# Optimization experiments

Measured on AMD Instinct MI355X. Metric: run time of the kernel, lower is better.

## Reference

```python
import jax, jax.numpy as jnp
import numpy as np

D = 2048      # feature dim (fc1 = Linear(2*2048, 2048))
S = 10240


def setup_inputs() -> dict:
    key = jax.random.key(0)
    ks = jax.random.split(key, 16)
    sc = 0.02
    z = lambda *s: jnp.zeros(s, jnp.float32)
    return {
        "x0": jax.random.normal(ks[0], (1, 1, D), jnp.float32),
        "x1": jax.random.normal(ks[1], (1, S, D), jnp.float32),
        # fc1: Linear(4096, 2048)  (stored input-major for x @ W)
        "W1": jax.random.normal(ks[2], (2 * D, D), jnp.float32) * sc,
        "b1": z(D),
        # fc2: Linear(2048, 1)
        "W2": jax.random.normal(ks[3], (D, 1), jnp.float32) * sc,
        "b2": z(1),
        # LSTM(input=1, hidden=1, bidirectional): per-direction gate params [4] = (i,f,g,o)
        "Wih_f": jax.random.normal(ks[4], (4,), jnp.float32) * 0.5,
        "Whh_f": jax.random.normal(ks[5], (4,), jnp.float32) * 0.5,
        "bih_f": z(4),
        "bhh_f": z(4),
        "Wih_b": jax.random.normal(ks[6], (4,), jnp.float32) * 0.5,
        "Whh_b": jax.random.normal(ks[7], (4,), jnp.float32) * 0.5,
        "bih_b": z(4),
        "bhh_b": z(4),
        # fc3: Linear(10, 1)
        "W3": jax.random.normal(ks[8], (10, 1), jnp.float32) * sc,
        "b3": z(1),
    }


def _lstm_dir(x_seq, Wih, Whh, bih, bhh):
    """Single-direction LSTM, input_size=hidden_size=1, batch=1.
    x_seq: [S] scalars. Returns h sequence [S]. PyTorch gate order (i,f,g,o)."""
    b = bih + bhh

    def step(carry, x):
        h, c = carry
        g = Wih * x + Whh * h + b              # [4]
        i = jax.nn.sigmoid(g[0])
        f = jax.nn.sigmoid(g[1])
        gg = jnp.tanh(g[2])
        o = jax.nn.sigmoid(g[3])
        c = f * c + i * gg
        h = o * jnp.tanh(c)
        return (h, c), h

    h0 = jnp.zeros((), x_seq.dtype)
    c0 = jnp.zeros((), x_seq.dtype)
    _, hs = jax.lax.scan(step, (h0, c0), x_seq)
    return hs


def reference(x0, x1, W1, b1, W2, b2,
              Wih_f, Whh_f, bih_f, bhh_f,
              Wih_b, Whh_b, bih_b, bhh_b,
              W3, b3):
    # similarity: cat(|x0 - x1|, x0 + x1) along features (x0 broadcasts over S)
    sim = jnp.concatenate([jnp.abs(x0 - x1), x0 + x1], axis=2)   # [1, S, 2D]
    h = jax.nn.relu(jnp.einsum('bsf,fd->bsd', sim, W1) + b1)     # [1, S, D]
    # (dropout is identity in eval mode)
    s = jax.nn.sigmoid(jnp.einsum('bsd,do->bso', h, W2) + b2)    # [1, S, 1]
    x_seq = s[0, :, 0]                                           # [S]

    h_f = _lstm_dir(x_seq, Wih_f, Whh_f, bih_f, bhh_f)           # [S]
    h_b = _lstm_dir(x_seq[::-1], Wih_b, Whh_b, bih_b, bhh_b)[::-1]
    out = jnp.stack([h_f, h_b], axis=1)                          # [S, 2] == lstm out [S,1,2]

    grp = out.reshape(1, -1, 10)                                 # [1, S*2/10, 10]
    y = jax.nn.sigmoid(grp @ W3 + b3)                            # [1, S*2/10, 1]
    return y.reshape(1, -1)
```

## Files before the change

### kernel.cpp

```cpp
#include <hip/hip_runtime.h>
#include <hip/hip_bf16.h>

#define DD 2048
#define SS 10240
#define KK 4096

typedef __bf16 bf16x8 __attribute__((ext_vector_type(8)));
typedef float  f32x4  __attribute__((ext_vector_type(4)));

__device__ __forceinline__ unsigned short f2bf_rne(float x) {
    unsigned int u = __float_as_uint(x);
    u += 0x7FFFu + ((u >> 16) & 1u);
    return (unsigned short)(u >> 16);
}

__global__ __launch_bounds__(256) void prep_sim_kernel(
    const float* __restrict__ W1, const float* __restrict__ b2,
    const float* __restrict__ x0, const float* __restrict__ x1,
    unsigned short* __restrict__ W1T, float* __restrict__ s_pre,
    unsigned short* __restrict__ simB) {
    __shared__ float tile[64][65];
    const int t = threadIdx.x;

    if (blockIdx.x < (KK / 64) * (DD / 64)) {
        const int bf = blockIdx.x % (KK / 64);
        const int bd = blockIdx.x / (KK / 64);
        const int f0 = bf * 64, d0 = bd * 64;
#pragma unroll
        for (int p = 0; p < 4; ++p) {
            int fr = p * 16 + (t >> 4);
            int dc = (t & 15) * 4;
            const float4 v = *(const float4*)&W1[(size_t)(f0 + fr) * DD + d0 + dc];
            tile[fr][dc + 0] = v.x; tile[fr][dc + 1] = v.y;
            tile[fr][dc + 2] = v.z; tile[fr][dc + 3] = v.w;
        }
        __syncthreads();
#pragma unroll
        for (int p = 0; p < 4; ++p) {
            int dr = p * 16 + (t >> 4);
            int fc = (t & 15) * 4;
            ushort4 o;
            o.x = f2bf_rne(tile[fc + 0][dr]);
            o.y = f2bf_rne(tile[fc + 1][dr]);
            o.z = f2bf_rne(tile[fc + 2][dr]);
            o.w = f2bf_rne(tile[fc + 3][dr]);
            *(ushort4*)&W1T[(size_t)(d0 + dr) * KK + f0 + fc] = o;
        }
        int gid = blockIdx.x * 256 + t;
        if (gid < SS) s_pre[gid] = b2[0];
    } else {
        const int s = blockIdx.x - (KK / 64) * (DD / 64);
        const int d = t * 8;
        const float4 a0 = *(const float4*)&x0[d];
        const float4 a1 = *(const float4*)&x0[d + 4];
        const float4 v0 = *(const float4*)&x1[(size_t)s * DD + d];
        const float4 v1 = *(const float4*)&x1[(size_t)s * DD + d + 4];
        ushort4 lo0, lo1, hi0, hi1;
        lo0.x = f2bf_rne(fabsf(a0.x - v0.x)); hi0.x = f2bf_rne(a0.x + v0.x);
        lo0.y = f2bf_rne(fabsf(a0.y - v0.y)); hi0.y = f2bf_rne(a0.y + v0.y);
        lo0.z = f2bf_rne(fabsf(a0.z - v0.z)); hi0.z = f2bf_rne(a0.z + v0.z);
        lo0.w = f2bf_rne(fabsf(a0.w - v0.w)); hi0.w = f2bf_rne(a0.w + v0.w);
        lo1.x = f2bf_rne(fabsf(a1.x - v1.x)); hi1.x = f2bf_rne(a1.x + v1.x);
        lo1.y = f2bf_rne(fabsf(a1.y - v1.y)); hi1.y = f2bf_rne(a1.y + v1.y);
        lo1.z = f2bf_rne(fabsf(a1.z - v1.z)); hi1.z = f2bf_rne(a1.z + v1.z);
        lo1.w = f2bf_rne(fabsf(a1.w - v1.w)); hi1.w = f2bf_rne(a1.w + v1.w);
        unsigned short* row = &simB[(size_t)s * KK];
        *(ushort4*)&row[d]          = lo0;
        *(ushort4*)&row[d + 4]      = lo1;
        *(ushort4*)&row[DD + d]     = hi0;
        *(ushort4*)&row[DD + d + 4] = hi1;
    }
}

#define BM3 320
#define BN3 256
#define BK3 64
#define NKT (KK / BK3)

#define STAGE_A(ktv, BUFV)                                                     \
    _Pragma("unroll")                                                          \
    for (int L = 0; L < 5; ++L) {                                              \
        __builtin_amdgcn_global_load_lds(                                      \
            (const __attribute__((address_space(1))) void*)(gA + (size_t)L * 64 * KK + (size_t)(ktv) * 64), \
            (__attribute__((address_space(3))) void*)&lds[BUFV][t * 8 + L * 4096], \
            16, 0, 0);                                                         \
    }
#define STAGE_B(ktv, BUFV)                                                     \
    _Pragma("unroll")                                                          \
    for (int L = 0; L < 4; ++L) {                                              \
        __builtin_amdgcn_global_load_lds(                                      \
            (const __attribute__((address_space(1))) void*)(gB + (size_t)L * 64 * KK + (size_t)(ktv) * 64), \
            (__attribute__((address_space(3))) void*)&lds[BUFV][20480 + t * 8 + L * 4096], \
            16, 0, 0);                                                         \
    }

#define BODY(ktv, BUF, SA_LIT, SB_LIT, DO_STAGE)                               \
    {                                                                          \
        asm volatile("s_waitcnt vmcnt(" SA_LIT ")" ::: "memory");              \
        __builtin_amdgcn_s_barrier();                                          \
        __builtin_amdgcn_sched_barrier(0);                                     \
        if (DO_STAGE) { STAGE_A((ktv) + 1, BUF ^ 1) }                          \
        asm volatile("s_waitcnt vmcnt(" SB_LIT ")" ::: "memory");              \
        __builtin_amdgcn_s_barrier();                                          \
        __builtin_amdgcn_sched_barrier(0);                                     \
        if (DO_STAGE) { STAGE_B((ktv) + 1, BUF ^ 1) }                          \
        _Pragma("unroll")                                                      \
        for (int ks = 0; ks < 2; ++ks) {                                       \
            const int gx = ks ? gx1 : gx0;                                     \
            bf16x8 afr[5], bfr[4];                                             \
            _Pragma("unroll")                                                  \
            for (int m = 0; m < 5; ++m)                                        \
                afr[m] = *(const bf16x8*)&lds[BUF][aoff + m * 1024 + gx];      \
            _Pragma("unroll")                                                  \
            for (int n = 0; n < 4; ++n)                                        \
                bfr[n] = *(const bf16x8*)&lds[BUF][boff + n * 1024 + gx];      \
            __builtin_amdgcn_s_barrier();                                      \
            __builtin_amdgcn_s_setprio(1);                                     \
            _Pragma("unroll")                                                  \
            for (int m = 0; m < 5; ++m)                                        \
                _Pragma("unroll")                                              \
                for (int n = 0; n < 4; ++n)                                    \
                    acc[m][n] = __builtin_amdgcn_mfma_f32_16x16x32_bf16(       \
                        afr[m], bfr[n], acc[m][n], 0, 0, 0);                   \
            __builtin_amdgcn_s_setprio(0);                                     \
            _Pragma("unroll")                                                  \
            for (int n = 0; n < 4; ++n)                                        \
                bfr[n] = *(const bf16x8*)&lds[BUF][boff + (4 + n) * 1024 + gx]; \
            __builtin_amdgcn_s_barrier();                                      \
            __builtin_amdgcn_s_setprio(1);                                     \
            _Pragma("unroll")                                                  \
            for (int m = 0; m < 5; ++m)                                        \
                _Pragma("unroll")                                              \
                for (int n = 0; n < 4; ++n)                                    \
                    acc[m][4 + n] = __builtin_amdgcn_mfma_f32_16x16x32_bf16(   \
                        afr[m], bfr[n], acc[m][4 + n], 0, 0, 0);               \
            __builtin_amdgcn_s_setprio(0);                                     \
        }                                                                      \
    }

__global__ __launch_bounds__(512, 2) void gemm3_kernel(
    const unsigned short* __restrict__ simB,
    const unsigned short* __restrict__ W1T,
    const float* __restrict__ b1, const float* __restrict__ W2,
    float* __restrict__ s_pre) {
    __shared__ unsigned short lds[2][36864];

    const int t    = threadIdx.x;
    const int lane = t & 63;
    const int wv   = t >> 6;
    const int wr   = wv >> 1;
    const int wc   = wv & 1;
    const int lr   = lane & 15;
    const int g4   = lane >> 4;
    const int l7   = lane & 7;

    const int bm = blockIdx.x & 31;
    const int bn = blockIdx.x >> 5;
    const int m0 = bm * BM3, n0 = bn * BN3;

    const int trow = t >> 3;
    const int gsrc = (t & 7) ^ (trow & 7);
    const unsigned short* gA = simB + (size_t)(m0 + trow) * KK + gsrc * 8;
    const unsigned short* gB = W1T  + (size_t)(n0 + trow) * KK + gsrc * 8;

    const int aoff = (wr * 80 + lr) * 64;
    const int boff = 20480 + (wc * 128 + lr) * 64;
    const int gx0  = ((0 * 4 + g4) ^ l7) * 8;
    const int gx1  = ((1 * 4 + g4) ^ l7) * 8;

    f32x4 acc[5][8];
#pragma unroll
    for (int m = 0; m < 5; ++m)
#pragma unroll
        for (int n = 0; n < 8; ++n)
            acc[m][n] = (f32x4){0.f, 0.f, 0.f, 0.f};

    STAGE_A(0, 0)
    STAGE_B(0, 0)

#pragma unroll 1
    for (int kt = 0; kt < NKT - 2; kt += 2) {
        BODY(kt,     0, "4", "5", 1)
        BODY(kt + 1, 1, "4", "5", 1)
    }
    BODY(NKT - 2, 0, "4", "5", 1)
    BODY(NKT - 1, 1, "4", "0", 0)

    float b1v[8], w2v[8];
#pragma unroll
    for (int n = 0; n < 8; ++n) {
        int col = n0 + wc * 128 + n * 16 + lr;
        b1v[n] = b1[col];
        w2v[n] = W2[col];
    }
#pragma unroll
    for (int m = 0; m < 5; ++m) {
#pragma unroll
        for (int r = 0; r < 4; ++r) {
            float rowsum = 0.f;
#pragma unroll
            for (int n = 0; n < 8; ++n) {
                float v = acc[m][n][r] + b1v[n];
                v = fmaxf(v, 0.f);
                rowsum = fmaf(v, w2v[n], rowsum);
            }
            rowsum += __shfl_xor(rowsum, 1);
            rowsum += __shfl_xor(rowsum, 2);
            rowsum += __shfl_xor(rowsum, 4);
            rowsum += __shfl_xor(rowsum, 8);
            if (lr == 0) {
                int row = m0 + wr * 80 + m * 16 + g4 * 4 + r;
                atomicAdd(&s_pre[row], rowsum);
            }
        }
    }
}

#define BM 128
#define BN 128
#define BK 32

__global__ __launch_bounds__(256) void gemm_kernel(
    const float* __restrict__ x0, const float* __restrict__ x1,
    const unsigned short* __restrict__ W1T,
    const float* __restrict__ b1, const float* __restrict__ W2,
    float* __restrict__ s_pre) {
    __shared__ unsigned short As[BM][BK];
    __shared__ unsigned short Bs[BN][BK];

    const int tid  = threadIdx.x;
    const int lane = tid & 63;
    const int wave = tid >> 6;
    const int wr = wave >> 1, wc = wave & 1;
    const int bm = blockIdx.x / (DD / BN);
    const int bn = blockIdx.x % (DD / BN);
    const int m0 = bm * BM, n0 = bn * BN;
    const int lr = lane & 15;
    const int lk = (lane >> 4) * 8;

    f32x4 acc[4][4];
#pragma unroll
    for (int m = 0; m < 4; ++m)
#pragma unroll
        for (int n = 0; n < 4; ++n)
            acc[m][n] = (f32x4){0.f, 0.f, 0.f, 0.f};

    for (int k0 = 0; k0 < KK; k0 += BK) {
        __syncthreads();
#pragma unroll
        for (int p = 0; p < 2; ++p) {
            int L  = tid + p * 256;
            int n  = L >> 2;
            int k8 = (L & 3) * 8;
            const unsigned short* g = &W1T[(size_t)(n0 + n) * KK + k0 + k8];
            unsigned short* l = &Bs[0][0] + (size_t)L * 8;
            __builtin_amdgcn_global_load_lds(
                (const __attribute__((address_space(1))) void*)g,
                (__attribute__((address_space(3))) void*)l, 16, 0, 0);
        }
        {
            const int f0 = k0 & (DD - 1);
            const bool second = (k0 >= DD);
            const int fc = (tid & 7) * 4;
            const float4 v0 = *(const float4*)&x0[f0 + fc];
#pragma unroll
            for (int p = 0; p < 4; ++p) {
                int row = p * 32 + (tid >> 3);
                const float4 v1 = *(const float4*)&x1[(size_t)(m0 + row) * DD + f0 + fc];
                ushort4 o;
                o.x = f2bf_rne(second ? (v0.x + v1.x) : fabsf(v0.x - v1.x));
                o.y = f2bf_rne(second ? (v0.y + v1.y) : fabsf(v0.y - v1.y));
                o.z = f2bf_rne(second ? (v0.z + v1.z) : fabsf(v0.z - v1.z));
                o.w = f2bf_rne(second ? (v0.w + v1.w) : fabsf(v0.w - v1.w));
                *(ushort4*)&As[row][fc] = o;
            }
        }
        __syncthreads();

        bf16x8 a[4], b[4];
#pragma unroll
        for (int m = 0; m < 4; ++m)
            a[m] = *(const bf16x8*)&As[wr * 64 + m * 16 + lr][lk];
#pragma unroll
        for (int n = 0; n < 4; ++n)
            b[n] = *(const bf16x8*)&Bs[wc * 64 + n * 16 + lr][lk];
#pragma unroll
        for (int m = 0; m < 4; ++m)
#pragma unroll
            for (int n = 0; n < 4; ++n)
                acc[m][n] = __builtin_amdgcn_mfma_f32_16x16x32_bf16(
                    a[m], b[n], acc[m][n], 0, 0, 0);
    }

    float b1v[4], w2v[4];
#pragma unroll
    for (int n = 0; n < 4; ++n) {
        int col = n0 + wc * 64 + n * 16 + lr;
        b1v[n] = b1[col];
        w2v[n] = W2[col];
    }
#pragma unroll
    for (int m = 0; m < 4; ++m) {
#pragma unroll
        for (int r = 0; r < 4; ++r) {
            float rowsum = 0.f;
#pragma unroll
            for (int n = 0; n < 4; ++n) {
                float v = acc[m][n][r] + b1v[n];
                v = fmaxf(v, 0.f);
                rowsum = fmaf(v, w2v[n], rowsum);
            }
            rowsum += __shfl_xor(rowsum, 1);
            rowsum += __shfl_xor(rowsum, 2);
            rowsum += __shfl_xor(rowsum, 4);
            rowsum += __shfl_xor(rowsum, 8);
            if (lr == 0) {
                int row = m0 + wr * 64 + m * 16 + (lane >> 4) * 4 + r;
                atomicAdd(&s_pre[row], rowsum);
            }
        }
    }
}

#define CHUNK 64
#define WARM  192
#define NCH   (SS / CHUNK)

__device__ __forceinline__ float sigf(float x) {
    return 1.f / (1.f + __expf(-x));
}
__device__ __forceinline__ float tanhfast(float x) {
    return 2.f / (1.f + __expf(-2.f * x)) - 1.f;
}

__global__ __launch_bounds__(64) void lstm_kernel(
    const float* __restrict__ s_pre,
    const float* __restrict__ Wih_f, const float* __restrict__ Whh_f,
    const float* __restrict__ bih_f, const float* __restrict__ bhh_f,
    const float* __restrict__ Wih_b, const float* __restrict__ Whh_b,
    const float* __restrict__ bih_b, const float* __restrict__ bhh_b,
    float* __restrict__ hf, float* __restrict__ hb) {
    int id = blockIdx.x * blockDim.x + threadIdx.x;
    if (id >= 2 * NCH) return;
    int dir = id / NCH;
    int ch  = id % NCH;
    const float* Wih = dir ? Wih_b : Wih_f;
    const float* Whh = dir ? Whh_b : Whh_f;
    const float* bih = dir ? bih_b : bih_f;
    const float* bhh = dir ? bhh_b : bhh_f;
    const float wi0 = Wih[0], wi1 = Wih[1], wi2 = Wih[2], wi3 = Wih[3];
    const float wh0 = Whh[0], wh1 = Whh[1], wh2 = Whh[2], wh3 = Whh[3];
    const float bb0 = bih[0] + bhh[0], bb1 = bih[1] + bhh[1];
    const float bb2 = bih[2] + bhh[2], bb3 = bih[3] + bhh[3];

    const int pout0 = ch * CHUNK;
    int pstart = pout0 - WARM; if (pstart < 0) pstart = 0;
    const int pend = pout0 + CHUNK;

    float h = 0.f, c = 0.f;
    for (int p4 = pstart; p4 < pend; p4 += 4) {
        float4 xv;
        if (dir == 0) {
            xv = *(const float4*)&s_pre[p4];
        } else {
            const float4 tv = *(const float4*)&s_pre[SS - 4 - p4];
            xv = (float4){tv.w, tv.z, tv.y, tv.x};
        }
        const bool wr_out = (p4 >= pout0);
        const float xa[4] = {xv.x, xv.y, xv.z, xv.w};
#pragma unroll
        for (int q = 0; q < 4; ++q) {
            const int p = p4 + q;
            float x  = sigf(xa[q]);
            float g0 = fmaf(wi0, x, fmaf(wh0, h, bb0));
            float g1 = fmaf(wi1, x, fmaf(wh1, h, bb1));
            float g2 = fmaf(wi2, x, fmaf(wh2, h, bb2));
            float g3 = fmaf(wi3, x, fmaf(wh3, h, bb3));
            float gi = sigf(g0);
            float gf = sigf(g1);
            float gg = tanhfast(g2);
            float go = sigf(g3);
            c = fmaf(gf, c, gi * gg);
            h = go * tanhfast(c);
            if (wr_out) {
                int s = dir ? (SS - 1 - p) : p;
                if (dir) hb[s] = h; else hf[s] = h;
            }
        }
    }
}

__global__ __launch_bounds__(256) void final_kernel(
    const float* __restrict__ hf, const float* __restrict__ hb,
    const float* __restrict__ W3, const float* __restrict__ b3,
    float* __restrict__ out) {
    int j = blockIdx.x * blockDim.x + threadIdx.x;
    if (j >= (SS * 2) / 10) return;
    float acc = b3[0];
#pragma unroll
    for (int i = 0; i < 5; ++i) {
        acc = fmaf(hf[5 * j + i], W3[2 * i],     acc);
        acc = fmaf(hb[5 * j + i], W3[2 * i + 1], acc);
    }
    out[j] = sigf(acc);
}

extern "C" void kernel_launch(void* const* d_in, const int* in_sizes, int n_in,
                              void* d_out, int out_size, void* d_ws, size_t ws_size,
                              hipStream_t stream) {
    const float* x0    = (const float*)d_in[0];
    const float* x1    = (const float*)d_in[1];
    const float* W1    = (const float*)d_in[2];
    const float* b1    = (const float*)d_in[3];
    const float* W2    = (const float*)d_in[4];
    const float* b2    = (const float*)d_in[5];
    const float* Wih_f = (const float*)d_in[6];
    const float* Whh_f = (const float*)d_in[7];
    const float* bih_f = (const float*)d_in[8];
    const float* bhh_f = (const float*)d_in[9];
    const float* Wih_b = (const float*)d_in[10];
    const float* Whh_b = (const float*)d_in[11];
    const float* bih_b = (const float*)d_in[12];
    const float* bhh_b = (const float*)d_in[13];
    const float* W3    = (const float*)d_in[14];
    const float* b3    = (const float*)d_in[15];
    float* out = (float*)d_out;

    char* ws = (char*)d_ws;
    const size_t w1t_bytes = (size_t)KK * DD * 2;
    unsigned short* W1T = (unsigned short*)ws;
    float* s_pre = (float*)(ws + w1t_bytes);
    float* hf    = s_pre + SS;
    float* hb    = hf + SS;
    size_t off_sim = w1t_bytes + 3 * (size_t)SS * 4;
    off_sim = (off_sim + 255) & ~(size_t)255;
    unsigned short* simB = (unsigned short*)(ws + off_sim);
    const size_t need = off_sim + (size_t)SS * KK * 2;

    if (ws_size >= need) {
        prep_sim_kernel<<<(KK / 64) * (DD / 64) + SS, 256, 0, stream>>>(
            W1, b2, x0, x1, W1T, s_pre, simB);
        gemm3_kernel<<<(SS / BM3) * (DD / BN3), 512, 0, stream>>>(
            simB, W1T, b1, W2, s_pre);
    } else {
        prep_sim_kernel<<<(KK / 64) * (DD / 64), 256, 0, stream>>>(
            W1, b2, x0, x1, W1T, s_pre, simB);
        gemm_kernel<<<(SS / BM) * (DD / BN), 256, 0, stream>>>(
            x0, x1, W1T, b1, W2, s_pre);
    }
    lstm_kernel<<<(2 * NCH + 63) / 64, 64, 0, stream>>>(
        s_pre, Wih_f, Whh_f, bih_f, bhh_f, Wih_b, Whh_b, bih_b, bhh_b, hf, hb);
    final_kernel<<<((SS * 2) / 10 + 255) / 256, 256, 0, stream>>>(hf, hb, W3, b3, out);
}
```

Baseline: 388.4 us.

## Switch GEMM to BK=32 with 4-stage LDS ring and 3-ahead prefetch

Halves the K-tile to 32, replaces the double-buffered A/B staging with a 4-deep LDS ring buffer and prefetches three tiles ahead using a unified per-thread load table with a new XOR swizzle. This deepens the pipeline so global-to-LDS latency is hidden behind more MFMA work, and drops one barrier/waitcnt pair per tile. In exchange there are twice as many K-iterations (more barriers per unit of work) and less MFMA work per barrier.

```diff
diff --git a/kernel.cpp b/kernel.cpp
--- a/kernel.cpp
+++ b/kernel.cpp
@@ -74,68 +74,57 @@
 
 #define BM3 320
 #define BN3 256
-#define BK3 64
+#define BK3 32
 #define NKT (KK / BK3)
-
-#define STAGE_A(ktv, BUFV)                                                     \
-    _Pragma("unroll")                                                          \
-    for (int L = 0; L < 5; ++L) {                                              \
-        __builtin_amdgcn_global_load_lds(                                      \
-            (const __attribute__((address_space(1))) void*)(gA + (size_t)L * 64 * KK + (size_t)(ktv) * 64), \
-            (__attribute__((address_space(3))) void*)&lds[BUFV][t * 8 + L * 4096], \
-            16, 0, 0);                                                         \
-    }
-#define STAGE_B(ktv, BUFV)                                                     \
-    _Pragma("unroll")                                                          \
-    for (int L = 0; L < 4; ++L) {                                              \
-        __builtin_amdgcn_global_load_lds(                                      \
-            (const __attribute__((address_space(1))) void*)(gB + (size_t)L * 64 * KK + (size_t)(ktv) * 64), \
-            (__attribute__((address_space(3))) void*)&lds[BUFV][20480 + t * 8 + L * 4096], \
-            16, 0, 0);                                                         \
-    }
-
-#define BODY(ktv, BUF, SA_LIT, SB_LIT, DO_STAGE)                               \
+#define BUFSZ 18432
+#define BBASE 10240
+
+#define STAGE(ktv)                                                             \
     {                                                                          \
-        asm volatile("s_waitcnt vmcnt(" SA_LIT ")" ::: "memory");              \
+        unsigned short* lbw = &lds[(ktv) & 3][0];                              \
+        _Pragma("unroll")                                                      \
+        for (int L = 0; L < 5; ++L)                                            \
+            __builtin_amdgcn_global_load_lds(                                  \
+                (const __attribute__((address_space(1))) void*)(gsrc[L] + (size_t)(ktv) * BK3), \
+                (__attribute__((address_space(3))) void*)(lbw + ldsoff[L]),    \
+                16, 0, 0);                                                     \
+    }
+
+#define BODY(ktv, VM_LIT, DO_STAGE)                                            \
+    {                                                                          \
+        asm volatile("s_waitcnt vmcnt(" VM_LIT ")" ::: "memory");              \
         __builtin_amdgcn_s_barrier();                                          \
         __builtin_amdgcn_sched_barrier(0);                                     \
-        if (DO_STAGE) { STAGE_A((ktv) + 1, BUF ^ 1) }                          \
-        asm volatile("s_waitcnt vmcnt(" SB_LIT ")" ::: "memory");              \
+        if (DO_STAGE) { STAGE((ktv) + 3) }                                     \
+        const unsigned short* lbr = &lds[(ktv) & 3][0];                        \
+        bf16x8 afr[5], bfr[4];                                                 \
+        _Pragma("unroll")                                                      \
+        for (int m = 0; m < 5; ++m)                                            \
+            afr[m] = *(const bf16x8*)&lbr[aoff + m * 512];                     \
+        _Pragma("unroll")                                                      \
+        for (int n = 0; n < 4; ++n)                                            \
+            bfr[n] = *(const bf16x8*)&lbr[boff + n * 512];                     \
         __builtin_amdgcn_s_barrier();                                          \
-        __builtin_amdgcn_sched_barrier(0);                                     \
-        if (DO_STAGE) { STAGE_B((ktv) + 1, BUF ^ 1) }                          \
-        _Pragma("unroll")                                                      \
-        for (int ks = 0; ks < 2; ++ks) {                                       \
-            const int gx = ks ? gx1 : gx0;                                     \
-            bf16x8 afr[5], bfr[4];                                             \
-            _Pragma("unroll")                                                  \
-            for (int m = 0; m < 5; ++m)                                        \
-                afr[m] = *(const bf16x8*)&lds[BUF][aoff + m * 1024 + gx];      \
+        __builtin_amdgcn_s_setprio(1);                                         \
+        _Pragma("unroll")                                                      \
+        for (int m = 0; m < 5; ++m)                                            \
             _Pragma("unroll")                                                  \
             for (int n = 0; n < 4; ++n)                                        \
-                bfr[n] = *(const bf16x8*)&lds[BUF][boff + n * 1024 + gx];      \
-            __builtin_amdgcn_s_barrier();                                      \
-            __builtin_amdgcn_s_setprio(1);                                     \
-            _Pragma("unroll")                                                  \
-            for (int m = 0; m < 5; ++m)                                        \
-                _Pragma("unroll")                                              \
-                for (int n = 0; n < 4; ++n)                                    \
-                    acc[m][n] = __builtin_amdgcn_mfma_f32_16x16x32_bf16(       \
-                        afr[m], bfr[n], acc[m][n], 0, 0, 0);                   \
-            __builtin_amdgcn_s_setprio(0);                                     \
+                acc[m][n] = __builtin_amdgcn_mfma_f32_16x16x32_bf16(           \
+                    afr[m], bfr[n], acc[m][n], 0, 0, 0);                       \
+        __builtin_amdgcn_s_setprio(0);                                         \
+        _Pragma("unroll")                                                      \
+        for (int n = 0; n < 4; ++n)                                            \
+            bfr[n] = *(const bf16x8*)&lbr[boff + (4 + n) * 512];               \
+        __builtin_amdgcn_s_barrier();                                          \
+        __builtin_amdgcn_s_setprio(1);                                         \
+        _Pragma("unroll")                                                      \
+        for (int m = 0; m < 5; ++m)                                            \
             _Pragma("unroll")                                                  \
             for (int n = 0; n < 4; ++n)                                        \
-                bfr[n] = *(const bf16x8*)&lds[BUF][boff + (4 + n) * 1024 + gx]; \
-            __builtin_amdgcn_s_barrier();                                      \
-            __builtin_amdgcn_s_setprio(1);                                     \
-            _Pragma("unroll")                                                  \
-            for (int m = 0; m < 5; ++m)                                        \
-                _Pragma("unroll")                                              \
-                for (int n = 0; n < 4; ++n)                                    \
-                    acc[m][4 + n] = __builtin_amdgcn_mfma_f32_16x16x32_bf16(   \
-                        afr[m], bfr[n], acc[m][4 + n], 0, 0, 0);               \
-            __builtin_amdgcn_s_setprio(0);                                     \
-        }                                                                      \
+                acc[m][4 + n] = __builtin_amdgcn_mfma_f32_16x16x32_bf16(       \
+                    afr[m], bfr[n], acc[m][4 + n], 0, 0, 0);                   \
+        __builtin_amdgcn_s_setprio(0);                                         \
     }
 
 __global__ __launch_bounds__(512, 2) void gemm3_kernel(
@@ -143,7 +132,7 @@
     const unsigned short* __restrict__ W1T,
     const float* __restrict__ b1, const float* __restrict__ W2,
     float* __restrict__ s_pre) {
-    __shared__ unsigned short lds[2][36864];
+    __shared__ unsigned short lds[4][BUFSZ];
 
     const int t    = threadIdx.x;
     const int lane = t & 63;
@@ -152,21 +141,51 @@
     const int wc   = wv & 1;
     const int lr   = lane & 15;
     const int g4   = lane >> 4;
-    const int l7   = lane & 7;
 
     const int bm = blockIdx.x & 31;
     const int bn = blockIdx.x >> 5;
     const int m0 = bm * BM3, n0 = bn * BN3;
 
-    const int trow = t >> 3;
-    const int gsrc = (t & 7) ^ (trow & 7);
-    const unsigned short* gA = simB + (size_t)(m0 + trow) * KK + gsrc * 8;
-    const unsigned short* gB = W1T  + (size_t)(n0 + trow) * KK + gsrc * 8;
-
-    const int aoff = (wr * 80 + lr) * 64;
-    const int boff = 20480 + (wc * 128 + lr) * 64;
-    const int gx0  = ((0 * 4 + g4) ^ l7) * 8;
-    const int gx1  = ((1 * 4 + g4) ^ l7) * 8;
+    const unsigned short* gsrc[5];
+    int ldsoff[5];
+    {
+#pragma unroll
+        for (int L = 0; L < 2; ++L) {
+            int row = L * 128 + (t >> 2);
+            int sg  = (t & 3) ^ ((row >> 1) & 3);
+            gsrc[L] = simB + (size_t)(m0 + row) * KK + sg * 8;
+            ldsoff[L] = L * 4096 + t * 8;
+        }
+        if (t < 256) {
+            int row = 256 + (t >> 2);
+            int sg  = (t & 3) ^ ((row >> 1) & 3);
+            gsrc[2] = simB + (size_t)(m0 + row) * KK + sg * 8;
+            ldsoff[2] = 8192 + t * 8;
+        } else {
+            int tt = t - 256;
+            int row = tt >> 2;
+            int sg  = (tt & 3) ^ ((row >> 1) & 3);
+            gsrc[2] = W1T + (size_t)(n0 + row) * KK + sg * 8;
+            ldsoff[2] = BBASE + tt * 8;
+        }
+        {
+            int row = 64 + (t >> 2);
+            int sg  = (t & 3) ^ ((row >> 1) & 3);
+            gsrc[3] = W1T + (size_t)(n0 + row) * KK + sg * 8;
+            ldsoff[3] = BBASE + 2048 + t * 8;
+        }
+        {
+            int tt = t & 255;
+            int row = 192 + (tt >> 2);
+            int sg  = (tt & 3) ^ ((row >> 1) & 3);
+            gsrc[4] = W1T + (size_t)(n0 + row) * KK + sg * 8;
+            ldsoff[4] = BBASE + 6144 + tt * 8;
+        }
+    }
+
+    const int gx   = (g4 ^ ((lr >> 1) & 3)) * 8;
+    const int aoff = (wr * 80 + lr) * 32 + gx;
+    const int boff = BBASE + (wc * 128 + lr) * 32 + gx;
 
     f32x4 acc[5][8];
 #pragma unroll
@@ -175,16 +194,21 @@
         for (int n = 0; n < 8; ++n)
             acc[m][n] = (f32x4){0.f, 0.f, 0.f, 0.f};
 
-    STAGE_A(0, 0)
-    STAGE_B(0, 0)
+    STAGE(0)
+    STAGE(1)
+    STAGE(2)
 
 #pragma unroll 1
-    for (int kt = 0; kt < NKT - 2; kt += 2) {
-        BODY(kt,     0, "4", "5", 1)
-        BODY(kt + 1, 1, "4", "5", 1)
-    }
-    BODY(NKT - 2, 0, "4", "5", 1)
-    BODY(NKT - 1, 1, "4", "0", 0)
+    for (int kt = 0; kt < NKT - 4; kt += 4) {
+        BODY(kt,     "10", 1)
+        BODY(kt + 1, "10", 1)
+        BODY(kt + 2, "10", 1)
+        BODY(kt + 3, "10", 1)
+    }
+    BODY(NKT - 4, "10", 1)
+    BODY(NKT - 3, "10", 0)
+    BODY(NKT - 2, "5",  0)
+    BODY(NKT - 1, "0",  0)
 
     float b1v[8], w2v[8];
 #pragma unroll
```

Measured after the change: 388.9 us. No clear change (+0.1%).
